# Optimization experiments

Measured on AMD Instinct MI355X. Metric: run time of the kernel, lower is better.

Reference implementation:

```python
import jax, jax.numpy as jnp
import numpy as np

B, C, H, W = 2, 16, 384, 384
ADJ = 1
HID = 64
N_ITERS = 8


def _to_c(x):
    return x[..., 0] + 1j * x[..., 1]


def _to_r(z):
    return jnp.stack([z.real, z.imag], axis=-1)


def fft2c(x):
    z = jnp.fft.ifftshift(_to_c(x), axes=(-2, -1))
    z = jnp.fft.fft2(z, axes=(-2, -1), norm='ortho')
    return _to_r(jnp.fft.fftshift(z, axes=(-2, -1)))


def ifft2c(x):
    z = jnp.fft.ifftshift(_to_c(x), axes=(-2, -1))
    z = jnp.fft.ifft2(z, axes=(-2, -1), norm='ortho')
    return _to_r(jnp.fft.fftshift(z, axes=(-2, -1)))


def complex_mul(a, b):
    ar, ai = a[..., 0], a[..., 1]
    br, bi = b[..., 0], b[..., 1]
    return jnp.stack([ar * br - ai * bi, ar * bi + ai * br], axis=-1)


def complex_conj(x):
    return jnp.stack([x[..., 0], -x[..., 1]], axis=-1)


def _conv(x, w, b):
    y = jax.lax.conv_general_dilated(x, w, (1, 1), 'SAME',
                                     dimension_numbers=('NCHW', 'OIHW', 'NCHW'))
    return y + b[None, :, None, None]


def sens_expand(x, sens_maps):
    # x: [b, adj, h, w, 2] -> repeat to coils, multiply, fft
    c = sens_maps.shape[1]
    x = jnp.repeat(x, c // ADJ, axis=1)
    return fft2c(complex_mul(x, sens_maps))


def sens_reduce(x, sens_maps):
    b, c, h, w, _ = x.shape
    x = ifft2c(x)
    x = complex_mul(x, complex_conj(sens_maps))
    return x.reshape(b, ADJ, c // ADJ, h, w, 2).sum(axis=2)  # [b, adj, h, w, 2]


def apply_model(x, w1, b1, w2, b2):
    # complex_to_chan_dim: [b, c, h, w, 2] -> [b, 2c, h, w]
    b, c, h, w, _ = x.shape
    x = jnp.transpose(x, (0, 4, 1, 2, 3)).reshape(b, 2 * c, h, w)
    # per-channel norm (torch std is unbiased -> ddof=1)
    xf = x.reshape(b, 2 * c, h * w)
    mean = xf.mean(axis=2)[:, :, None, None]
    std = jnp.std(xf, axis=2, ddof=1)[:, :, None, None]
    xn = (x - mean) / std
    # regularizer model (2-layer conv)
    y = _conv(jax.nn.relu(_conv(xn, w1, b1)), w2, b2)
    y = y * std + mean
    # chan_complex_to_last_dim
    return jnp.transpose(y.reshape(b, 2, c, h, w), (0, 2, 3, 4, 1))


def mask_predictor(x, w_mp, b_mp):
    # x: [b, 2, h, w] -> prob over width columns [b, 1, w]
    feat = x.mean(axis=2)  # [b, 2, w]
    logits = jnp.einsum('bcw,c->bw', feat, w_mp) + b_mp
    return jax.nn.softmax(logits, axis=-1)[:, None, :]


def update_mask(current_mask, pred_prob, add_list, it_idx):
    # batched variable-k top-k scatter (fused version of the per-sample loop)
    p = pred_prob[:, :, None, :, None] * (1.0 - current_mask)  # [b,1,1,w,1]
    b = p.shape[0]
    pv = p.reshape(b, -1)                       # [b, w]
    order = jnp.argsort(-pv, axis=-1)           # descending
    ranks = jnp.argsort(order, axis=-1)         # rank of each column
    add_num = add_list[:, it_idx]               # [b]
    add = (ranks < add_num[:, None]).astype(current_mask.dtype)
    return current_mask + add[:, None, None, :, None]


def setup_inputs():
    key = jax.random.key(0)
    ks = jax.random.split(key, 10)
    return {
        'current_kspace': jax.random.normal(ks[0], (B, C, H, W, 2), jnp.float32),
        'ref_kspace': jax.random.normal(ks[1], (B, C, H, W, 2), jnp.float32),
        'mask': jax.random.randint(ks[2], (B, 1, 1, W, 1), 0, 2).astype(bool),
        'sens_maps': jax.random.normal(ks[3], (B, C, H, W, 2), jnp.float32) / np.sqrt(C),
        'it_idx': 3,
        'current_mask': jnp.zeros((B, 1, 1, W, 1), jnp.float32),
        'current_prob': jax.random.uniform(ks[4], (B, 1, W), jnp.float32),
        'add_list': jax.random.randint(ks[5], (B, N_ITERS), 1, 30),
        'dc_weight': jnp.ones((1,), jnp.float32),
        'w1': jax.random.normal(ks[6], (HID, 2 * ADJ, 3, 3), jnp.float32) * 0.05,
        'b1': jnp.zeros((HID,), jnp.float32),
        'w2': jax.random.normal(ks[7], (2 * ADJ, HID, 3, 3), jnp.float32) * 0.05,
        'b2': jnp.zeros((2 * ADJ,), jnp.float32),
        'w_mp': jax.random.normal(ks[8], (2,), jnp.float32) * 0.1,
        'b_mp': jnp.zeros((), jnp.float32),
    }


def reference(current_kspace, ref_kspace, mask, sens_maps, it_idx, current_mask,
              current_prob, add_list, dc_weight, w1, b1, w2, b2, w_mp, b_mp):
    restore_im = apply_model(sens_reduce(current_kspace, sens_maps), w1, b1, w2, b2)
    model_term = sens_expand(restore_im, sens_maps)
    soft_dc = jnp.where(mask, model_term - ref_kspace, 0.0) * dc_weight
    pred_kspace = model_term - soft_dc
    restore_im_dc = sens_reduce(pred_kspace, sens_maps)
    # [b, h, w, 2] -> fft2c -> [b, 2, h, w]
    kim = jnp.transpose(fft2c(restore_im_dc[:, 0]), (0, 3, 1, 2))
    pred_prob = mask_predictor(kim, w_mp, b_mp)
    pred_mask = update_mask(current_mask, pred_prob, add_list, it_idx)
    return pred_kspace, pred_mask, pred_prob
```

## Files before the change

### kernel.cpp

```cpp
#include <hip/hip_runtime.h>
#include <hip/hip_bf16.h>
#include <math.h>

#define HH 384
#define WW 384
#define NPIX (HH*WW)
#define BB 2
#define CC 16
#define NKF 9437184

__device__ inline float2 cmul(float2 a, float2 b) {
    return make_float2(a.x*b.x - a.y*b.y, a.x*b.y + a.y*b.x);
}
__device__ inline float bf2f(unsigned short u) {
    union { unsigned int i; float f; } c; c.i = ((unsigned)u) << 16; return c.f;
}
__device__ inline float2 loadc2(const void* p, int dt, size_t i) {
    if (dt == 1) { ushort2 u = ((const ushort2*)p)[i];
        return make_float2(bf2f(u.x), bf2f(u.y)); }
    if (dt == 2) { double2 d = ((const double2*)p)[i];
        return make_float2((float)d.x, (float)d.y); }
    return ((const float2*)p)[i];
}
__device__ inline float loads1(const void* p, int dt, size_t i) {
    if (dt == 1) return bf2f(((const unsigned short*)p)[i]);
    if (dt == 2) return (float)((const double*)p)[i];
    return ((const float*)p)[i];
}
__device__ inline int flex_int1(const void* p) {
    unsigned v = ((const unsigned*)p)[0];
    if (v < 1000000u) return (int)v;
    float f = ((const float*)p)[0];
    if (f > -1e6f && f < 1e6f && f == floorf(f)) return (int)f;
    return (int)((const double*)p)[0];
}
__device__ inline int flex_int_arr(const void* p, int i) {
    const unsigned* u = (const unsigned*)p;
    if (u[1] == 0u && u[3] == 0u) return (int)u[2*i];
    if (u[0] >= 1u && u[0] < 1000000u) return (int)u[i];
    float f = ((const float*)p)[i];
    if (f > -1e6f && f < 1e6f) return (int)f;
    return (int)((const double*)p)[i];
}

__global__ void detect_dtype(const unsigned* __restrict__ q, int* dt)
{
    __shared__ int bad, sig;
    if (threadIdx.x == 0) { bad = 0; sig = 0; }
    __syncthreads();
    const unsigned short* q16 = (const unsigned short*)q;
    int mybad = 0, mysig = 0;
    for (int i = threadIdx.x; i < 8192; i += 256) {
        unsigned short u = q16[i];
        int e = (u >> 7) & 0xFF;
        if (!(e == 0 || (e >= 100 && e <= 140))) mybad++;
    }
    for (int i = threadIdx.x; i < 2048; i += 256) {
        unsigned hi = q[2*i + 1];
        int e = (hi >> 20) & 0x7FF;
        if (e >= 1003 && e <= 1040) mysig++;
    }
    atomicAdd(&bad, mybad);
    atomicAdd(&sig, mysig);
    __syncthreads();
    if (threadIdx.x == 0)
        *dt = (bad < 400) ? 1 : ((sig > 1950) ? 2 : 0);
}

#define SP 385

template<int DIR, int AXIS, int MODE, int NL>
__global__ __launch_bounds__(512)
void fft384(const void* in, float2* out, const int* DTp, int srcExt,
            const void* aux1, const void* aux2,
            const int* FLAGp, const void* dcwp, float2* outk)
{
    __shared__ float2 tw[384];
    __shared__ float2 stage[NL * SP];
    const int tid = threadIdx.x;
    const int dt = (srcExt || MODE) ? *DTp : 0;
    for (int j = tid; j < 384; j += 512) {
        float s, c;
        sincosf(-6.283185307179586f * (float)j / 384.0f, &s, &c);
        tw[j] = make_float2(c, s);
    }
    const int BPI = 384 / NL;
    const int img = blockIdx.x / BPI;
    const int t0  = (blockIdx.x % BPI) * NL;
    const size_t base = (size_t)img * NPIX;
    float2* dst = out + base;

    if (AXIS == 0) {
        if (MODE == 1) {
            const float2* rim = (const float2*)aux1;
            const size_t rbase = (size_t)(img >> 4) * NPIX;
            for (int f = tid; f < NL*384; f += 512) {
                int l = f / 384, n = f - l*384;
                size_t pix = (size_t)(t0 + l)*384 + n;
                stage[l*SP + n] = cmul(rim[rbase + pix], loadc2(aux2, dt, base + pix));
            }
        } else {
            for (int f = tid; f < NL*384; f += 512) {
                int l = f / 384, n = f - l*384;
                stage[l*SP + n] = loadc2(in, dt, base + (size_t)(t0 + l)*384 + n);
            }
        }
    } else {
        for (int f = tid; f < NL*384; f += 512) {
            int l = f & (NL-1), n = f / NL;
            stage[l*SP + n] = loadc2(in, dt, base + (size_t)n*384 + (t0 + l));
        }
    }
    __syncthreads();

    const int g    = tid >> 6;
    const int lane = tid & 63;
    const float SCALE = 0.05103103630798288f;

    #pragma unroll
    for (int it = 0; it < NL/8; ++it) {
        const int l = it*8 + g;
        float2* w = &stage[l*SP];

        float2 v6[6];
        #pragma unroll
        for (int m = 0; m < 6; ++m) v6[m] = w[lane + 64*m];
        __builtin_amdgcn_wave_barrier();
        #pragma unroll
        for (int m = 0; m < 6; ++m) {
            int n = lane + 64*m;
            float sgn = (n & 1) ? -1.f : 1.f;
            int q = n / 3;
            int r3 = n - 3*q;
            w[r3*128 + q] = make_float2(v6[m].x*sgn, v6[m].y*sgn);
        }
        __builtin_amdgcn_wave_barrier();

        #pragma unroll
        for (int s = 0; s < 7; ++s) {
            const int h = 64 >> s;
            const int tstep = 3 << s;
            const int j = lane & (h-1);
            const int i = ((lane & ~(h-1)) << 1) | j;
            float2 t = tw[j * tstep];
            if (DIR < 0) t.y = -t.y;
            #pragma unroll
            for (int n1 = 0; n1 < 3; ++n1) {
                float2* a = w + (n1 << 7);
                float2 u = a[i], vv = a[i+h];
                float2 d = make_float2(u.x - vv.x, u.y - vv.y);
                a[i]   = make_float2(u.x + vv.x, u.y + vv.y);
                a[i+h] = cmul(d, t);
            }
            __builtin_amdgcn_wave_barrier();
        }

        float2 A0[2], A1[2], A2[2];
        #pragma unroll
        for (int half = 0; half < 2; ++half) {
            int k2 = lane + 64*half;
            int r  = __brev((unsigned)k2) >> 25;
            A0[half] = w[r]; A1[half] = w[128 + r]; A2[half] = w[256 + r];
        }
        __builtin_amdgcn_wave_barrier();
        #pragma unroll
        for (int half = 0; half < 2; ++half) {
            int k2 = lane + 64*half;
            float2 t1 = tw[k2];
            float2 t2 = tw[(2*k2) % 384];
            float2 w3 = tw[128], w3b = tw[256];
            if (DIR < 0) { t1.y=-t1.y; t2.y=-t2.y; w3.y=-w3.y; w3b.y=-w3b.y; }
            float2 b1 = cmul(A1[half], t1), b2 = cmul(A2[half], t2);
            float2 a0 = A0[half];
            float2 X0 = make_float2(a0.x + b1.x + b2.x, a0.y + b1.y + b2.y);
            float2 c1 = cmul(w3, b1), c2 = cmul(w3b, b2);
            float2 X1 = make_float2(a0.x + c1.x + c2.x, a0.y + c1.y + c2.y);
            float2 d1 = cmul(w3b, b1), d2 = cmul(w3, b2);
            float2 X2 = make_float2(a0.x + d1.x + d2.x, a0.y + d1.y + d2.y);
            float sc = (k2 & 1) ? -SCALE : SCALE;
            w[k2      ] = make_float2(X0.x*sc, X0.y*sc);
            w[k2 + 128] = make_float2(X1.x*sc, X1.y*sc);
            w[k2 + 256] = make_float2(X2.x*sc, X2.y*sc);
        }
        __builtin_amdgcn_wave_barrier();
    }
    __syncthreads();

    if (AXIS == 0) {
        for (int f = tid; f < NL*384; f += 512) {
            int l = f / 384, n = f - l*384;
            dst[(size_t)(t0 + l)*384 + n] = stage[l*SP + n];
        }
    } else {
        if (MODE == 2) {
            const int fl = *FLAGp;
            const float dw = loads1(dcwp, dt, 0);
            const int bb = img >> 4;
            for (int f = tid; f < NL*384; f += 512) {
                int l = f & (NL-1), n = f / NL;
                int wcol = t0 + l;
                size_t pix = (size_t)n*384 + wcol;
                float2 v = stage[l*SP + n];
                int m;
                switch (fl) {
                    case 0:  m = ((const unsigned char*)aux2)[bb*384 + wcol] != 0; break;
                    case 4:  m = ((const unsigned short*)aux2)[bb*384 + wcol] != 0; break;
                    case 3:  m = ((const unsigned long long*)aux2)[bb*384 + wcol] != 0ULL; break;
                    default: m = ((const unsigned int*)aux2)[bb*384 + wcol] != 0u; break;
                }
                if (m) {
                    float2 r = loadc2(aux1, dt, base + pix);
                    v.x -= (v.x - r.x)*dw;
                    v.y -= (v.y - r.y)*dw;
                }
                outk[base + pix] = v;
            }
        } else {
            for (int f = tid; f < NL*384; f += 512) {
                int l = f & (NL-1), n = f / NL;
                dst[(size_t)n*384 + (t0 + l)] = stage[l*SP + n];
            }
        }
    }
}

__global__ void detect_mask(const unsigned char* __restrict__ m, int* flag)
{
    __shared__ int sA, sB, sC, sD, sE;
    if (threadIdx.x == 0) { sA = sB = sC = sD = sE = 0; }
    __syncthreads();
    for (int i = threadIdx.x; i < 768; i += 256) {
        unsigned char v = m[i];
        if (v > 1) atomicOr(&sA, 1);
        if ((i & 3) && v) atomicOr(&sB, 1);
    }
    const unsigned short* m16 = (const unsigned short*)m;
    for (int i = threadIdx.x; i < 384; i += 256)
        if (!(i & 1) && m16[i]) atomicOr(&sC, 1);
    const unsigned int* m32 = (const unsigned int*)m;
    for (int i = threadIdx.x; i < 192; i += 256) {
        if ((i & 1) && m32[i]) atomicOr(&sD, 1);
        if (!(i & 1) && m32[i]) atomicOr(&sE, 1);
    }
    __syncthreads();
    if (threadIdx.x == 0) {
        int f;
        if (!sA) { if (sB) f = 0; else if (sD) f = 2; else f = 3; }
        else     { if (sC) f = 4; else if (sE) f = 2; else f = 3; }
        *flag = f;
    }
}

template<bool WITH_STATS>
__global__ __launch_bounds__(256)
void reduce_sens(const float2* __restrict__ xin, const void* __restrict__ sens,
                 float2* __restrict__ ximg, const int* DTp,
                 float* __restrict__ partials)
{
    const int dt = *DTp;
    const int b = blockIdx.y;
    const int p = blockIdx.x*256 + threadIdx.x;
    float2 acc = make_float2(0.f, 0.f);
    for (int c = 0; c < CC; ++c) {
        size_t o = ((size_t)(b*CC + c))*NPIX + p;
        float2 a = xin[o];
        float2 s = loadc2(sens, dt, o);
        acc.x += a.x*s.x + a.y*s.y;
        acc.y += a.y*s.x - a.x*s.y;
    }
    ximg[(size_t)b*NPIX + p] = acc;
    if (WITH_STATS) {
        float sx = acc.x, sy = acc.y, qx = acc.x*acc.x, qy = acc.y*acc.y;
        #pragma unroll
        for (int o = 32; o > 0; o >>= 1) {
            sx += __shfl_down(sx, o, 64); sy += __shfl_down(sy, o, 64);
            qx += __shfl_down(qx, o, 64); qy += __shfl_down(qy, o, 64);
        }
        __shared__ float red[4][4];
        const int wv = threadIdx.x >> 6, lane = threadIdx.x & 63;
        if (lane == 0) {
            red[wv][0] = sx; red[wv][1] = sy; red[wv][2] = qx; red[wv][3] = qy;
        }
        __syncthreads();
        if (threadIdx.x == 0) {
            float t0 = red[0][0]+red[1][0]+red[2][0]+red[3][0];
            float t1 = red[0][1]+red[1][1]+red[2][1]+red[3][1];
            float t2 = red[0][2]+red[1][2]+red[2][2]+red[3][2];
            float t3 = red[0][3]+red[1][3]+red[2][3]+red[3][3];
            float* dst = partials + ((size_t)b*576 + blockIdx.x)*4;
            dst[0] = t0; dst[1] = t1; dst[2] = t2; dst[3] = t3;
        }
    }
}

__global__ __launch_bounds__(256)
void stats_finalize(const float* __restrict__ partials, float* __restrict__ ms)
{
    const int b = blockIdx.x;
    const int tid = threadIdx.x;
    float sx=0.f, sy=0.f, qx=0.f, qy=0.f;
    for (int i = tid; i < 576; i += 256) {
        const float* p = partials + ((size_t)b*576 + i)*4;
        sx += p[0]; sy += p[1]; qx += p[2]; qy += p[3];
    }
    __shared__ float r0[256], r1[256], r2[256], r3[256];
    r0[tid]=sx; r1[tid]=sy; r2[tid]=qx; r3[tid]=qy;
    __syncthreads();
    for (int s = 128; s > 0; s >>= 1) {
        if (tid < s) {
            r0[tid]+=r0[tid+s]; r1[tid]+=r1[tid+s];
            r2[tid]+=r2[tid+s]; r3[tid]+=r3[tid+s];
        }
        __syncthreads();
    }
    if (tid == 0) {
        const float N = (float)NPIX;
        float var0 = (r2[0] - r0[0]*r0[0]/N) / (N - 1.f);
        float var1 = (r3[0] - r1[0]*r1[0]/N) / (N - 1.f);
        ms[(b*2+0)*2]   = r0[0]/N;
        ms[(b*2+0)*2+1] = sqrtf(var0);
        ms[(b*2+1)*2]   = r1[0]/N;
        ms[(b*2+1)*2+1] = sqrtf(var1);
    }
}

__global__ __launch_bounds__(256)
void conv_fused(const float2* __restrict__ ximg, const void* __restrict__ w1g,
                const void* __restrict__ b1g, const void* __restrict__ w2g,
                const void* __restrict__ b2g, const float* __restrict__ msg,
                float2* __restrict__ rim, const int* DTp)
{
    __shared__ float2 inP[20][21];
    __shared__ float w1s[1152];
    __shared__ float w2s[1152];
    __shared__ float b1s[64];
    __shared__ float2 hidw[4][18*20];
    __shared__ float2 accs[4][256];

    const int dt = *DTp;
    const int b = blockIdx.z, bx = blockIdx.x, by = blockIdx.y;
    const int tid = threadIdx.x;
    const int wv = tid >> 6, lane = tid & 63;

    for (int f = tid; f < 1152; f += 256) {
        w1s[f] = loads1(w1g, dt, f);
        w2s[f] = loads1(w2g, dt, f);
    }
    if (tid < 64) b1s[tid] = loads1(b1g, dt, tid);
    const float mean0 = msg[(b*2+0)*2], istd0 = 1.f/msg[(b*2+0)*2+1];
    const float mean1 = msg[(b*2+1)*2], istd1 = 1.f/msg[(b*2+1)*2+1];
    for (int f = tid; f < 400; f += 256) {
        int yy = f / 20, xx = f - yy*20;
        int gy = by*16 + yy - 2, gx = bx*16 + xx - 2;
        float a = 0.f, c = 0.f;
        if (gy >= 0 && gy < HH && gx >= 0 && gx < WW) {
            float2 v = ximg[(size_t)b*NPIX + gy*WW + gx];
            a = (v.x - mean0)*istd0;
            c = (v.y - mean1)*istd1;
        }
        inP[yy][xx] = make_float2(a, c);
    }
    __syncthreads();

    float a0[4] = {0.f,0.f,0.f,0.f}, a1[4] = {0.f,0.f,0.f,0.f};
    float2* hid = hidw[wv];

    const int c1col = lane % 18;
    const int c1g   = lane / 18;
    const int c1y0  = 6 * c1g;
    const int tx = lane & 15, ybase = (lane >> 4) * 4;

    for (int j = 0; j < 8; ++j) {
        const int oa = wv*16 + 2*j;
        const float* wa = &w1s[oa*18];
        const float* wb = &w1s[(oa+1)*18];
        const float boa = b1s[oa], bob = b1s[oa+1];
        if (c1g < 3) {
            float2 r0c0 = inP[c1y0][c1col],   r0c1 = inP[c1y0][c1col+1],   r0c2 = inP[c1y0][c1col+2];
            float2 r1c0 = inP[c1y0+1][c1col], r1c1 = inP[c1y0+1][c1col+1], r1c2 = inP[c1y0+1][c1col+2];
            #pragma unroll
            for (int rr = 0; rr < 6; ++rr) {
                float2 r2c0 = inP[c1y0+rr+2][c1col];
                float2 r2c1 = inP[c1y0+rr+2][c1col+1];
                float2 r2c2 = inP[c1y0+rr+2][c1col+2];
                float accA = boa
                    + wa[0]*r0c0.x + wa[1]*r0c1.x + wa[2]*r0c2.x
                    + wa[3]*r1c0.x + wa[4]*r1c1.x + wa[5]*r1c2.x
                    + wa[6]*r2c0.x + wa[7]*r2c1.x + wa[8]*r2c2.x
                    + wa[9]*r0c0.y  + wa[10]*r0c1.y + wa[11]*r0c2.y
                    + wa[12]*r1c0.y + wa[13]*r1c1.y + wa[14]*r1c2.y
                    + wa[15]*r2c0.y + wa[16]*r2c1.y + wa[17]*r2c2.y;
                float accB = bob
                    + wb[0]*r0c0.x + wb[1]*r0c1.x + wb[2]*r0c2.x
                    + wb[3]*r1c0.x + wb[4]*r1c1.x + wb[5]*r1c2.x
                    + wb[6]*r2c0.x + wb[7]*r2c1.x + wb[8]*r2c2.x
                    + wb[9]*r0c0.y  + wb[10]*r0c1.y + wb[11]*r0c2.y
                    + wb[12]*r1c0.y + wb[13]*r1c1.y + wb[14]*r1c2.y
                    + wb[15]*r2c0.y + wb[16]*r2c1.y + wb[17]*r2c2.y;
                int hy = c1y0 + rr;
                int gy = by*16 + hy - 1, gx = bx*16 + c1col - 1;
                bool inb = (gy >= 0 && gy < HH && gx >= 0 && gx < WW);
                hid[hy*20 + c1col] = inb
                    ? make_float2(fmaxf(accA, 0.f), fmaxf(accB, 0.f))
                    : make_float2(0.f, 0.f);
                r0c0 = r1c0; r0c1 = r1c1; r0c2 = r1c2;
                r1c0 = r2c0; r1c1 = r2c1; r1c2 = r2c2;
            }
        }
        __builtin_amdgcn_wave_barrier();
        {
            const float* pa0 = &w2s[oa*9];
            const float* pa1 = &w2s[(oa+1)*9];
            const float* pb0 = &w2s[576 + oa*9];
            const float* pb1 = &w2s[576 + (oa+1)*9];
            float2 h00 = hid[ybase*20 + tx],     h01 = hid[ybase*20 + tx+1],     h02 = hid[ybase*20 + tx+2];
            float2 h10 = hid[(ybase+1)*20 + tx], h11 = hid[(ybase+1)*20 + tx+1], h12 = hid[(ybase+1)*20 + tx+2];
            #pragma unroll
            for (int r = 0; r < 4; ++r) {
                float2 h20 = hid[(ybase+r+2)*20 + tx];
                float2 h21 = hid[(ybase+r+2)*20 + tx+1];
                float2 h22 = hid[(ybase+r+2)*20 + tx+2];
                a0[r] += pa0[0]*h00.x + pa0[1]*h01.x + pa0[2]*h02.x
                       + pa0[3]*h10.x + pa0[4]*h11.x + pa0[5]*h12.x
                       + pa0[6]*h20.x + pa0[7]*h21.x + pa0[8]*h22.x
                       + pa1[0]*h00.y + pa1[1]*h01.y + pa1[2]*h02.y
                       + pa1[3]*h10.y + pa1[4]*h11.y + pa1[5]*h12.y
                       + pa1[6]*h20.y + pa1[7]*h21.y + pa1[8]*h22.y;
                a1[r] += pb0[0]*h00.x + pb0[1]*h01.x + pb0[2]*h02.x
                       + pb0[3]*h10.x + pb0[4]*h11.x + pb0[5]*h12.x
                       + pb0[6]*h20.x + pb0[7]*h21.x + pb0[8]*h22.x
                       + pb1[0]*h00.y + pb1[1]*h01.y + pb1[2]*h02.y
                       + pb1[3]*h10.y + pb1[4]*h11.y + pb1[5]*h12.y
                       + pb1[6]*h20.y + pb1[7]*h21.y + pb1[8]*h22.y;
                h00 = h10; h01 = h11; h02 = h12;
                h10 = h20; h11 = h21; h12 = h22;
            }
        }
        __builtin_amdgcn_wave_barrier();
    }
    #pragma unroll
    for (int r = 0; r < 4; ++r)
        accs[wv][(ybase + r)*16 + tx] = make_float2(a0[r], a1[r]);
    __syncthreads();
    {
        const int p = tid;
        float s0 = loads1(b2g, dt, 0), s1 = loads1(b2g, dt, 1);
        #pragma unroll
        for (int wvi = 0; wvi < 4; ++wvi) {
            s0 += accs[wvi][p].x;
            s1 += accs[wvi][p].y;
        }
        const float std0 = msg[(b*2+0)*2+1], std1 = msg[(b*2+1)*2+1];
        int ty = p >> 4, txx = p & 15;
        rim[(size_t)b*NPIX + (by*16+ty)*WW + (bx*16+txx)]
            = make_float2(s0*std0 + mean0, s1*std1 + mean1);
    }
}

__global__ __launch_bounds__(384)
void predictor(const float2* __restrict__ kimg, const void* __restrict__ wmp,
               const void* __restrict__ bmp, float* __restrict__ prob,
               float* __restrict__ outp, const int* DTp)
{
    const int dt = *DTp;
    const int b = blockIdx.x, w = threadIdx.x;
    float s0 = 0.f, s1 = 0.f;
    for (int h = 0; h < HH; ++h) {
        float2 v = kimg[((size_t)b*HH + h)*WW + w];
        s0 += v.x; s1 += v.y;
    }
    float logit = (s0*loads1(wmp,dt,0) + s1*loads1(wmp,dt,1)) * (1.0f/384.0f)
                + loads1(bmp,dt,0);
    __shared__ float red[8];
    float m = logit;
    for (int o = 32; o > 0; o >>= 1) m = fmaxf(m, __shfl_down(m, o, 64));
    int wid = w >> 6, lane = w & 63;
    if (lane == 0) red[wid] = m;
    __syncthreads();
    if (w == 0) { float mm = red[0]; for (int i = 1; i < 6; ++i) mm = fmaxf(mm, red[i]); red[6] = mm; }
    __syncthreads();
    m = red[6];
    float e = expf(logit - m);
    float s = e;
    for (int o = 32; o > 0; o >>= 1) s += __shfl_down(s, o, 64);
    __syncthreads();
    if (lane == 0) red[wid] = s;
    __syncthreads();
    if (w == 0) { float ss = 0.f; for (int i = 0; i < 6; ++i) ss += red[i]; red[7] = ss; }
    __syncthreads();
    float pr = e / red[7];
    prob[b*WW + w] = pr;
    outp[b*WW + w] = pr;
}

__global__ __launch_bounds__(384)
void update_mask_k(const float* __restrict__ prob, const void* __restrict__ cmask,
                   const void* __restrict__ add_list, const void* __restrict__ itp,
                   float* __restrict__ outm, const int* DTp)
{
    const int dt = *DTp;
    const int b = blockIdx.x, w = threadIdx.x;
    __shared__ float p[384];
    float cm = loads1(cmask, dt, b*WW + w);
    float pv = prob[b*WW + w] * (1.0f - cm);
    p[w] = pv;
    __syncthreads();
    int rank = 0;
    for (int i = 0; i < 384; ++i) {
        float q = p[i];
        rank += (q > pv) || (q == pv && i < w);
    }
    int it = flex_int1(itp);
    if (it < 0 || it > 7) it = 0;
    int addn = flex_int_arr(add_list, b*8 + it);
    float val = cm + ((rank < addn) ? 1.0f : 0.0f);
    outm[b*WW + w] = val;
}

extern "C" void kernel_launch(void* const* d_in, const int* in_sizes, int n_in,
                              void* d_out, int out_size, void* d_ws, size_t ws_size,
                              hipStream_t stream)
{
    const void* src  = d_in[0];
    const void* tgt  = d_in[1];
    const void* mask = d_in[2];
    const void* sens = d_in[3];
    const void* itp  = d_in[4];
    const void* cmask= d_in[5];
    const void* addl = d_in[7];
    const void* dcw  = d_in[8];
    const void* w1   = d_in[9];
    const void* b1   = d_in[10];
    const void* w2   = d_in[11];
    const void* b2   = d_in[12];
    const void* wmp  = d_in[13];
    const void* bmp  = d_in[14];
    float* out = (float*)d_out;

    float* ws = (float*)d_ws;
    const size_t OFF_XIMG = 9437184;
    const size_t OFF_RIM  = OFF_XIMG + 589824;
    const size_t OFF_MS   = OFF_RIM  + 589824;
    const size_t OFF_PROB = OFF_MS + 8;
    const size_t OFF_FLAG = OFF_PROB + 768;
    const size_t OFF_DT   = OFF_FLAG + 4;
    const size_t OFF_PART = OFF_DT + 4;

    float2* A    = (float2*)ws;
    float2* XIMG = (float2*)(ws + OFF_XIMG);
    float2* RIM  = (float2*)(ws + OFF_RIM);
    float*  MS   = ws + OFF_MS;
    float*  PROB = ws + OFF_PROB;
    int*    FLAG = (int*)(ws + OFF_FLAG);
    int*    DT   = (int*)(ws + OFF_DT);
    float*  PART = ws + OFF_PART;

    const int gRow    = (BB*CC)*48;
    const int gCol    = (BB*CC)*24;
    const int gSmallR = BB*48;
    const int gSmallC = BB*24;

    detect_dtype<<<1, 256, 0, stream>>>((const unsigned*)src, DT);
    detect_mask<<<1, 256, 0, stream>>>((const unsigned char*)mask, FLAG);

    fft384<-1,0,0,8><<<gRow, 512, 0, stream>>>(src, A, DT, 1, nullptr, nullptr, nullptr, nullptr, nullptr);
    fft384<-1,1,0,16><<<gCol, 512, 0, stream>>>(A, A, DT, 0, nullptr, nullptr, nullptr, nullptr, nullptr);
    reduce_sens<true><<<dim3((NPIX/256), BB), 256, 0, stream>>>(A, sens, XIMG, DT, PART);
    stats_finalize<<<BB, 256, 0, stream>>>(PART, MS);

    conv_fused<<<dim3(24,24,BB), 256, 0, stream>>>(XIMG, w1, b1, w2, b2, MS, RIM, DT);

    fft384<1,0,1,8><<<gRow, 512, 0, stream>>>(nullptr, A, DT, 0, RIM, sens, nullptr, nullptr, nullptr);
    fft384<1,1,2,16><<<gCol, 512, 0, stream>>>(A, A, DT, 0, tgt, mask, FLAG, dcw, (float2*)out);

    fft384<-1,0,0,8><<<gRow, 512, 0, stream>>>(out, A, DT, 0, nullptr, nullptr, nullptr, nullptr, nullptr);
    fft384<-1,1,0,16><<<gCol, 512, 0, stream>>>(A, A, DT, 0, nullptr, nullptr, nullptr, nullptr, nullptr);
    reduce_sens<false><<<dim3((NPIX/256), BB), 256, 0, stream>>>(A, sens, XIMG, DT, nullptr);

    fft384<1,0,0,8><<<gSmallR, 512, 0, stream>>>(XIMG, XIMG, DT, 0, nullptr, nullptr, nullptr, nullptr, nullptr);
    fft384<1,1,0,16><<<gSmallC, 512, 0, stream>>>(XIMG, XIMG, DT, 0, nullptr, nullptr, nullptr, nullptr, nullptr);

    predictor<<<BB, 384, 0, stream>>>(XIMG, wmp, bmp, PROB, out + 9437184 + 768, DT);
    update_mask_k<<<BB, 384, 0, stream>>>(PROB, cmask, addl, itp, out + 9437184, DT);
}
```

Baseline: 329.7 us.

## Split conv hidden channels across two blocks and fold partial sums into FFT load

The fused conv kernel now splits the 64 hidden channels into two halves, launching twice as many blocks, each writing an unscaled partial output to a separate buffer. The following row-FFT kernel loads both partials, adds the second-layer bias and undoes the normalization before the sensitivity multiply. This doubles the conv grid to raise occupancy and parallelism on a small 1152-block launch, at the cost of an extra image-sized buffer and extra reads in the FFT prologue.

```diff
diff --git a/kernel.cpp b/kernel.cpp
--- a/kernel.cpp
+++ b/kernel.cpp
@@ -93,11 +93,20 @@
     if (AXIS == 0) {
         if (MODE == 1) {
             const float2* rim = (const float2*)aux1;
-            const size_t rbase = (size_t)(img >> 4) * NPIX;
+            const int bb = img >> 4;
+            const size_t rbase = (size_t)bb * NPIX;
+            const float* msgf = (const float*)outk;
+            const float b20 = loads1(dcwp, dt, 0), b21 = loads1(dcwp, dt, 1);
+            const float mean0 = msgf[(bb*2+0)*2], std0 = msgf[(bb*2+0)*2+1];
+            const float mean1 = msgf[(bb*2+1)*2], std1 = msgf[(bb*2+1)*2+1];
             for (int f = tid; f < NL*384; f += 512) {
                 int l = f / 384, n = f - l*384;
                 size_t pix = (size_t)(t0 + l)*384 + n;
-                stage[l*SP + n] = cmul(rim[rbase + pix], loadc2(aux2, dt, base + pix));
+                float2 p1 = rim[rbase + pix];
+                float2 p2 = rim[(size_t)BB*NPIX + rbase + pix];
+                float2 y = make_float2((p1.x + p2.x + b20)*std0 + mean0,
+                                       (p1.y + p2.y + b21)*std1 + mean1);
+                stage[l*SP + n] = cmul(y, loadc2(aux2, dt, base + pix));
             }
         } else {
             for (int f = tid; f < NL*384; f += 512) {
@@ -338,7 +347,10 @@
     __shared__ float2 accs[4][256];
 
     const int dt = *DTp;
-    const int b = blockIdx.z, bx = blockIdx.x, by = blockIdx.y;
+    const int z = blockIdx.z;
+    const int b = z >> 1, half = z & 1;
+    const int chbase = half * 32;
+    const int bx = blockIdx.x, by = blockIdx.y;
     const int tid = threadIdx.x;
     const int wv = tid >> 6, lane = tid & 63;
 
@@ -370,8 +382,8 @@
     const int c1y0  = 6 * c1g;
     const int tx = lane & 15, ybase = (lane >> 4) * 4;
 
-    for (int j = 0; j < 8; ++j) {
-        const int oa = wv*16 + 2*j;
+    for (int j = 0; j < 4; ++j) {
+        const int oa = chbase + wv*8 + 2*j;
         const float* wa = &w1s[oa*18];
         const float* wb = &w1s[(oa+1)*18];
         const float boa = b1s[oa], bob = b1s[oa+1];
@@ -444,16 +456,15 @@
     __syncthreads();
     {
         const int p = tid;
-        float s0 = loads1(b2g, dt, 0), s1 = loads1(b2g, dt, 1);
+        float s0 = 0.f, s1 = 0.f;
         #pragma unroll
         for (int wvi = 0; wvi < 4; ++wvi) {
             s0 += accs[wvi][p].x;
             s1 += accs[wvi][p].y;
         }
-        const float std0 = msg[(b*2+0)*2+1], std1 = msg[(b*2+1)*2+1];
         int ty = p >> 4, txx = p & 15;
-        rim[(size_t)b*NPIX + (by*16+ty)*WW + (bx*16+txx)]
-            = make_float2(s0*std0 + mean0, s1*std1 + mean1);
+        rim[((size_t)half*BB + b)*NPIX + (size_t)(by*16+ty)*WW + (bx*16+txx)]
+            = make_float2(s0, s1);
     }
 }
 
@@ -540,7 +551,7 @@
     float* ws = (float*)d_ws;
     const size_t OFF_XIMG = 9437184;
     const size_t OFF_RIM  = OFF_XIMG + 589824;
-    const size_t OFF_MS   = OFF_RIM  + 589824;
+    const size_t OFF_MS   = OFF_RIM  + 2*589824;
     const size_t OFF_PROB = OFF_MS + 8;
     const size_t OFF_FLAG = OFF_PROB + 768;
     const size_t OFF_DT   = OFF_FLAG + 4;
@@ -568,9 +579,9 @@
     reduce_sens<true><<<dim3((NPIX/256), BB), 256, 0, stream>>>(A, sens, XIMG, DT, PART);
     stats_finalize<<<BB, 256, 0, stream>>>(PART, MS);
 
-    conv_fused<<<dim3(24,24,BB), 256, 0, stream>>>(XIMG, w1, b1, w2, b2, MS, RIM, DT);
-
-    fft384<1,0,1,8><<<gRow, 512, 0, stream>>>(nullptr, A, DT, 0, RIM, sens, nullptr, nullptr, nullptr);
+    conv_fused<<<dim3(24,24,BB*2), 256, 0, stream>>>(XIMG, w1, b1, w2, b2, MS, RIM, DT);
+
+    fft384<1,0,1,8><<<gRow, 512, 0, stream>>>(nullptr, A, DT, 0, RIM, sens, nullptr, b2, (float2*)MS);
     fft384<1,1,2,16><<<gCol, 512, 0, stream>>>(A, A, DT, 0, tgt, mask, FLAG, dcw, (float2*)out);
 
     fft384<-1,0,0,8><<<gRow, 512, 0, stream>>>(out, A, DT, 0, nullptr, nullptr, nullptr, nullptr, nullptr);
```

Measured after the change: 325.8 us. Within noise of the previous version (-1.2%).
